# Kernel optimization log

Hardware: AMD Instinct MI355X
Metric: run time of the kernel (lower is better)

Reference implementation:

```python
import jax, jax.numpy as jnp
import numpy as np

N_GRAPHS = 1250
NEG_SLOPE = 0.2

def gat_layer(x, src, dst, W, a_src, a_dst, b, concat):
    # x: [N, Fin]; W: [Fin, H*C]; a_src/a_dst: [H, C]; b: [H*C] or [C]
    N = x.shape[0]
    H, C = a_src.shape
    h = (x @ W).reshape(N, H, C)                      # [N,H,C]
    alpha_s = jnp.sum(h * a_src[None], axis=-1)       # [N,H]
    alpha_d = jnp.sum(h * a_dst[None], axis=-1)       # [N,H]
    e = jax.nn.leaky_relu(alpha_s[src] + alpha_d[dst], NEG_SLOPE)  # [E,H]
    # segment softmax over incoming edges of each target node
    m = jax.ops.segment_max(e, dst, num_segments=N)   # [N,H]
    m = jnp.where(jnp.isfinite(m), m, 0.0)
    ex = jnp.exp(e - m[dst])
    s = jax.ops.segment_sum(ex, dst, num_segments=N)  # [N,H]
    alpha = ex / (s[dst] + 1e-16)                     # [E,H]
    msg = h[src] * alpha[..., None]                   # [E,H,C]
    out = jax.ops.segment_sum(msg, dst, num_segments=N)  # [N,H,C]
    out = out.reshape(N, H * C) if concat else out.mean(axis=1)
    return out + b

def setup_inputs() -> dict:
    key = jax.random.key(0)
    ks = jax.random.split(key, 13)
    N, E = 50000, 100000
    x = jax.random.normal(ks[0], (N, 78), dtype=jnp.float32)
    edge_index = jax.random.randint(ks[1], (2, E), 0, N, dtype=jnp.int64)
    # sorted segment ids -> every graph non-empty (~40 nodes each)
    batch = jnp.sort(jax.random.randint(ks[2], (N,), 0, N_GRAPHS, dtype=jnp.int64))
    g = lambda k, shape, fan: jax.random.normal(k, shape, dtype=jnp.float32) / np.float32(np.sqrt(fan))
    return {
        'x': x, 'edge_index': edge_index, 'batch': batch,
        'W1': g(ks[3], (78, 780), 78), 'a_src1': g(ks[4], (10, 78), 78), 'a_dst1': g(ks[5], (10, 78), 78),
        'b1': jnp.zeros((780,), jnp.float32),
        'W2': g(ks[6], (780, 128), 780), 'a_src2': g(ks[7], (1, 128), 128), 'a_dst2': g(ks[8], (1, 128), 128),
        'b2': jnp.zeros((128,), jnp.float32),
        'fc_w': g(ks[9], (128, 128), 128), 'fc_b': jnp.zeros((128,), jnp.float32),
    }

def reference(x, edge_index, batch, W1, a_src1, a_dst1, b1, W2, a_src2, a_dst2, b2, fc_w, fc_b):
    N = x.shape[0]
    loop = jnp.arange(N, dtype=edge_index.dtype)
    src = jnp.concatenate([edge_index[0], loop])  # add self loops (PyG default)
    dst = jnp.concatenate([edge_index[1], loop])
    # dropout layers are identity in eval mode
    h = jax.nn.elu(gat_layer(x, src, dst, W1, a_src1, a_dst1, b1, concat=True))   # [N,780]
    h = jax.nn.relu(gat_layer(h, src, dst, W2, a_src2, a_dst2, b2, concat=True))  # [N,128]
    g = jax.ops.segment_max(h, batch, num_segments=N_GRAPHS)                      # [G,128]
    g = jnp.where(jnp.isfinite(g), g, 0.0)
    return jax.nn.relu(g @ fc_w + fc_b)
```

## Files before the change

kernel.cpp:

```cpp
#include <hip/hip_runtime.h>
#include <hip/hip_bf16.h>
#include <cstdint>

#define CAP 32
typedef __hip_bfloat16 bf16;
typedef __attribute__((ext_vector_type(8))) short short8;
typedef __attribute__((ext_vector_type(4))) float f32x4;

__device__ __forceinline__ float sb2f(short s) {
  unsigned int u = ((unsigned int)(unsigned short)s) << 16;
  return __uint_as_float(u);
}
__device__ __forceinline__ short f2sb(float f) {
  bf16 h = __float2bfloat16(f);
  return *reinterpret_cast<short*>(&h);
}


__device__ __forceinline__ void edge_sd(const int* __restrict__ ei, int e, int f,
                                        int& src, int& dst) {
  if (e < 100000) {
    if (f) { src = ei[2 * e]; dst = ei[200000 + 2 * e]; }
    else   { src = ei[e];     dst = ei[100000 + e]; }
  } else { src = dst = e - 100000; }
  src = min(max(src, 0), 49999);
  dst = min(max(dst, 0), 49999);
}

__global__ void k_prep(const float* __restrict__ x, const float* __restrict__ W1,
                       const float* __restrict__ W2, const float* __restrict__ aw1,
                       const float* __restrict__ dw1, bf16* __restrict__ xb,
                       bf16* __restrict__ W1t, bf16* __restrict__ W2t,
                       bf16* __restrict__ Wat, float* __restrict__ zp, int zeroWords) {
  int i = blockIdx.x * 256 + threadIdx.x;
  if (i < zeroWords) zp[i] = 0.f;
  const int n_xbv = 50000 * 12;
  const int n_w1 = 832 * 96;
  const int n_w2 = 128 * 832;
  const int n_wa = 32 * 96;
  if (i < n_xbv) {
    int r = i / 12, kg = i - r * 12;
    const float* xr = x + (size_t)r * 78;
    const int k0 = kg * 8;
    short8 ov;
#pragma unroll
    for (int c = 0; c < 8; c++) {
      int k = k0 + c;
      ov[c] = f2sb(k < 78 ? xr[k] : 0.f);
    }
    *(short8*)((short*)xb + (size_t)r * 96 + k0) = ov;
  } else if (i < n_xbv + n_w1) {
    int jdx = i - n_xbv;
    int np = jdx / 96, k = jdx - np * 96;
    int h = np / 80, j = np - h * 80;
    float v = 0.f;
    if (k < 78 && np < 800 && j < 78) v = W1[k * 780 + (h * 78 + j)];
    W1t[jdx] = __float2bfloat16(v);
  } else if (i < n_xbv + n_w1 + n_w2) {
    int jdx = i - n_xbv - n_w1;
    int c = jdx / 832, kp = jdx - c * 832;
    int h = kp / 80, j = kp - h * 80;
    float v = 0.f;
    if (kp < 800 && j < 78) v = W2[(h * 78 + j) * 128 + c];
    W2t[jdx] = __float2bfloat16(v);
  } else if (i < n_xbv + n_w1 + n_w2 + n_wa) {
    int jdx = i - n_xbv - n_w1 - n_w2;
    int c = jdx / 96, k = jdx - c * 96;
    float s = 0.f;
    if (k < 78 && c < 20) {
      const float* w = (c < 10) ? aw1 : dw1;
      int h = (c < 10) ? c : c - 10;
      const float* wrow = W1 + k * 780 + h * 78;
      const float* arow = w + h * 78;
      for (int q = 0; q < 78; q++) s += wrow[q] * arow[q];
    }
    Wat[c * 96 + k] = __float2bfloat16(s);
  }
}

__global__ __launch_bounds__(256) void k_gemm1(const bf16* __restrict__ xb,
                                               const bf16* __restrict__ W1t,
                                               const bf16* __restrict__ Wat,
                                               const float* __restrict__ b1,
                                               bf16* __restrict__ H1,
                                               float* __restrict__ as1,
                                               float* __restrict__ ad1) {
  __shared__ __align__(16) short Als[64 * 104];
  __shared__ __align__(16) short Bls[64 * 104];
  __shared__ __align__(16) short Wls[32 * 104];
  __shared__ __align__(16) float Cls[64 * 68];
  __shared__ float b1s[832];
  const int t = threadIdx.x;
  const int w = t >> 6, l = t & 63, l15 = l & 15, q = l >> 4;
  const int rowBase = blockIdx.x * 64;
  for (int s = t; s < 768; s += 256) {
    int row = s / 12, kg = s - row * 12;
    short8 v = {};
    int gr = rowBase + row;
    if (gr < 50000) v = *(const short8*)((const short*)xb + (size_t)gr * 96 + kg * 8);
    *(short8*)&Als[row * 104 + kg * 8] = v;
  }
  for (int s = t; s < 384; s += 256) {
    int row = s / 12, kg = s - row * 12;
    *(short8*)&Wls[row * 104 + kg * 8] =
        *(const short8*)((const short*)Wat + (size_t)row * 96 + kg * 8);
  }
  for (int s = t; s < 832; s += 256) {
    int h = s / 80, j = s - h * 80;
    b1s[s] = (s < 800 && j < 78) ? b1[h * 78 + j] : 0.f;
  }
  short8 breg[3];
  int bn[3], bk[3];
#pragma unroll
  for (int i = 0; i < 3; i++) {
    int s = t + i * 256;
    bn[i] = s / 12; bk[i] = s - bn[i] * 12;
    breg[i] = *(const short8*)((const short*)W1t + (size_t)bn[i] * 96 + bk[i] * 8);
  }
  for (int cc = 0; cc < 13; cc++) {
    __syncthreads();
#pragma unroll
    for (int i = 0; i < 3; i++) *(short8*)&Bls[bn[i] * 104 + bk[i] * 8] = breg[i];
    if (cc < 12) {
#pragma unroll
      for (int i = 0; i < 3; i++)
        breg[i] = *(const short8*)((const short*)W1t +
                                   (size_t)((cc + 1) * 64 + bn[i]) * 96 + bk[i] * 8);
    }
    __syncthreads();
    f32x4 acc[4] = {};
#pragma unroll
    for (int ks = 0; ks < 3; ks++) {
      short8 a = *(const short8*)&Als[(w * 16 + l15) * 104 + ks * 32 + q * 8];
#pragma unroll
      for (int nt = 0; nt < 4; nt++) {
        short8 b = *(const short8*)&Bls[(nt * 16 + l15) * 104 + ks * 32 + q * 8];
        acc[nt] = __builtin_amdgcn_mfma_f32_16x16x32_bf16(a, b, acc[nt], 0, 0, 0);
      }
    }
    __syncthreads();
#pragma unroll
    for (int nt = 0; nt < 4; nt++)
#pragma unroll
      for (int r = 0; r < 4; r++)
        Cls[(w * 16 + q * 4 + r) * 68 + nt * 16 + l15] = acc[nt][r];
    __syncthreads();
    {
      int r = t >> 2, c0 = (t & 3) * 16;
      int gr = rowBase + r;
      if (gr < 50000) {
        short8 o0, o1;
#pragma unroll
        for (int c = 0; c < 8; c++) o0[c] = f2sb(Cls[r * 68 + c0 + c] + b1s[cc * 64 + c0 + c]);
#pragma unroll
        for (int c = 0; c < 8; c++) o1[c] = f2sb(Cls[r * 68 + c0 + 8 + c] + b1s[cc * 64 + c0 + 8 + c]);
        short* dst = (short*)H1 + (size_t)gr * 832 + cc * 64 + c0;
        *(short8*)dst = o0;
        *(short8*)(dst + 8) = o1;
      }
    }
  }
  f32x4 acc2[2] = {};
#pragma unroll
  for (int ks = 0; ks < 3; ks++) {
    short8 a = *(const short8*)&Als[(w * 16 + l15) * 104 + ks * 32 + q * 8];
#pragma unroll
    for (int nt = 0; nt < 2; nt++) {
      short8 b = *(const short8*)&Wls[(nt * 16 + l15) * 104 + ks * 32 + q * 8];
      acc2[nt] = __builtin_amdgcn_mfma_f32_16x16x32_bf16(a, b, acc2[nt], 0, 0, 0);
    }
  }
  const int gr0 = rowBase + w * 16 + q * 4;
#pragma unroll
  for (int nt = 0; nt < 2; nt++) {
    int c = nt * 16 + l15;
#pragma unroll
    for (int r = 0; r < 4; r++) {
      int gr = gr0 + r;
      if (gr < 50000) {
        if (c < 10)       as1[gr * 10 + c] = acc2[nt][r];
        else if (c < 20)  ad1[gr * 10 + (c - 10)] = acc2[nt][r];
      }
    }
  }
}

__global__ void k_scatter(const int* __restrict__ ei, int* __restrict__ cnt,
                          int* __restrict__ csr, int* __restrict__ flag) {
  __shared__ int sf;
  const int t = threadIdx.x;
  if (t == 0) sf = 0;
  __syncthreads();
  int v = 0;
  for (int i = 1 + 2 * t; i < 2000; i += 512) v |= ei[i];
  if (v) atomicOr(&sf, 1);
  __syncthreads();
  const int f = (sf == 0) ? 1 : 0;
  if (blockIdx.x == 0 && t == 0) flag[0] = f;
  int e = blockIdx.x * 256 + t;
  if (e >= 150000) return;
  int src, dst;
  edge_sd(ei, e, f, src, dst);
  int pos = atomicAdd(&cnt[dst], 1);
  if (pos < CAP) csr[dst * CAP + pos] = src;
}

__global__ __launch_bounds__(256) void k_agg1(const bf16* __restrict__ H1,
                                              const float* __restrict__ as1,
                                              const float* __restrict__ ad1,
                                              const int* __restrict__ csr,
                                              const int* __restrict__ cnt,
                                              bf16* __restrict__ HL2) {
  __shared__ float sexw[2][CAP * 10];
  __shared__ float sden[2][16];
  __shared__ int ssrc[2][CAP];
  __shared__ int scnt[2];
  const int t = threadIdx.x;
  const int sub = t >> 7, tt = t & 127;
  const int n = blockIdx.x * 2 + sub;
  if (t < 2) scnt[t] = min(cnt[blockIdx.x * 2 + t], CAP);
  if (t >= 32 && t < 64) { int z = t - 32; sden[z >> 4][z & 15] = 0.f; }
  __syncthreads();
  const int cn = scnt[sub];
  if (tt < cn) ssrc[sub][tt] = csr[n * CAP + tt];
  __syncthreads();
  for (int wv = tt; wv < cn * 10; wv += 128) {
    int k = wv / 10, h = wv - k * 10;
    int src = ssrc[sub][k];
    float e = as1[src * 10 + h] + ad1[n * 10 + h];
    e = e >= 0.f ? e : 0.2f * e;
    float ex = __expf(e);
    sexw[sub][wv] = ex;
    atomicAdd(&sden[sub][h], ex);
  }
  __syncthreads();
  if (tt < 100) {
    const int head = tt / 10;
    const int j0 = tt * 8;
    float acc[8] = {};
    const float* sw = sexw[sub] + head;
    const short* H1s = (const short*)H1;
    for (int k = 0; k < cn; k++) {
      int src = ssrc[sub][k];
      short8 hv = *(const short8*)(H1s + (size_t)src * 832 + j0);
      float wk = sw[k * 10];
#pragma unroll
      for (int c = 0; c < 8; c++) acc[c] += wk * sb2f(hv[c]);
    }
    const float r0 = 1.f / (sden[sub][head] + 1e-16f);
    short8 ov;
#pragma unroll
    for (int c = 0; c < 8; c++) {
      float v = acc[c] * r0;
      v = v > 0.f ? v : __expf(v) - 1.f;
      ov[c] = f2sb(v);
    }
    *(short8*)((short*)HL2 + (size_t)n * 832 + j0) = ov;
  } else if (tt < 104) {
    short8 z = {};
    *(short8*)((short*)HL2 + (size_t)n * 832 + tt * 8) = z;
  }
}

__global__ __launch_bounds__(256) void k_gemm2(const bf16* __restrict__ A,
                                               const bf16* __restrict__ W2t,
                                               const float* __restrict__ AW2,
                                               const float* __restrict__ DW2,
                                               bf16* __restrict__ H2,
                                               float* __restrict__ as2,
                                               float* __restrict__ ad2) {
  __shared__ __align__(16) short Als[64 * 72];
  __shared__ __align__(16) short Bls[128 * 72];
  __shared__ float sAW[128], sDW[128];
  __shared__ float sS[4][64], sD[4][64];
  const int t = threadIdx.x;
  const int w = t >> 6, l = t & 63, l15 = l & 15, q = l >> 4;
  const int rowBase = blockIdx.x * 64;
  if (t < 128) sAW[t] = AW2[t];
  else         sDW[t - 128] = DW2[t - 128];
  const int ar = t >> 2, ak = t & 3;
  short8 areg[2], breg[4];
  {
    int gr0 = rowBase + ar;
#pragma unroll
    for (int i = 0; i < 2; i++) {
      short8 v = {};
      int gr = gr0;
      if (gr < 50000)
        v = *(const short8*)((const short*)A + (size_t)gr * 832 + 0 + (ak * 2 + i) * 8);
      areg[i] = v;
    }
#pragma unroll
    for (int i = 0; i < 4; i++) {
      int s = t + i * 256;
      int col = s >> 3, kg = s & 7;
      breg[i] = *(const short8*)((const short*)W2t + (size_t)col * 832 + 0 + kg * 8);
    }
  }
  f32x4 acc[4][2] = {};
  for (int kb = 0; kb < 832; kb += 64) {
    __syncthreads();
#pragma unroll
    for (int i = 0; i < 2; i++)
      *(short8*)&Als[ar * 72 + (ak * 2 + i) * 8] = areg[i];
#pragma unroll
    for (int i = 0; i < 4; i++) {
      int s = t + i * 256;
      int col = s >> 3, kg = s & 7;
      *(short8*)&Bls[col * 72 + kg * 8] = breg[i];
    }
    if (kb < 768) {
      int kn = kb + 64;
      int gr = rowBase + ar;
#pragma unroll
      for (int i = 0; i < 2; i++) {
        short8 v = {};
        if (gr < 50000)
          v = *(const short8*)((const short*)A + (size_t)gr * 832 + kn + (ak * 2 + i) * 8);
        areg[i] = v;
      }
#pragma unroll
      for (int i = 0; i < 4; i++) {
        int s = t + i * 256;
        int col = s >> 3, kg = s & 7;
        breg[i] = *(const short8*)((const short*)W2t + (size_t)col * 832 + kn + kg * 8);
      }
    }
    __syncthreads();
#pragma unroll
    for (int ks = 0; ks < 2; ks++) {
      short8 a[4];
#pragma unroll
      for (int mt = 0; mt < 4; mt++)
        a[mt] = *(const short8*)&Als[(mt * 16 + l15) * 72 + ks * 32 + q * 8];
#pragma unroll
      for (int ntl = 0; ntl < 2; ntl++) {
        short8 b = *(const short8*)&Bls[((w * 2 + ntl) * 16 + l15) * 72 + ks * 32 + q * 8];
#pragma unroll
        for (int mt = 0; mt < 4; mt++)
          acc[mt][ntl] = __builtin_amdgcn_mfma_f32_16x16x32_bf16(a[mt], b, acc[mt][ntl], 0, 0, 0);
      }
    }
  }
  const int col0 = w * 32 + l15, col1 = col0 + 16;
  const float aw0 = sAW[col0], aw1 = sAW[col1];
  const float dw0 = sDW[col0], dw1 = sDW[col1];
  f32x4 sp[4], dp[4];
#pragma unroll
  for (int mt = 0; mt < 4; mt++) {
    sp[mt] = acc[mt][0] * aw0 + acc[mt][1] * aw1;
    dp[mt] = acc[mt][0] * dw0 + acc[mt][1] * dw1;
  }
#pragma unroll
  for (int m = 1; m < 16; m <<= 1) {
#pragma unroll
    for (int mt = 0; mt < 4; mt++)
#pragma unroll
      for (int r = 0; r < 4; r++) {
        sp[mt][r] += __shfl_xor(sp[mt][r], m, 64);
        dp[mt][r] += __shfl_xor(dp[mt][r], m, 64);
      }
  }
  if (l15 == 0) {
#pragma unroll
    for (int mt = 0; mt < 4; mt++)
#pragma unroll
      for (int r = 0; r < 4; r++) {
        sS[w][mt * 16 + q * 4 + r] = sp[mt][r];
        sD[w][mt * 16 + q * 4 + r] = dp[mt][r];
      }
  }
#pragma unroll
  for (int mt = 0; mt < 4; mt++) {
    int gr0 = rowBase + mt * 16 + q * 4;
#pragma unroll
    for (int ntl = 0; ntl < 2; ntl++) {
      int gc = w * 32 + ntl * 16 + l15;
#pragma unroll
      for (int r = 0; r < 4; r++) {
        int gr = gr0 + r;
        if (gr < 50000) H2[(size_t)gr * 128 + gc] = __float2bfloat16(acc[mt][ntl][r]);
      }
    }
  }
  __syncthreads();
  if (t < 64) {
    int gr = rowBase + t;
    if (gr < 50000) as2[gr] = sS[0][t] + sS[1][t] + sS[2][t] + sS[3][t];
  } else if (t < 128) {
    int r2 = t - 64;
    int gr = rowBase + r2;
    if (gr < 50000) ad2[gr] = sD[0][r2] + sD[1][r2] + sD[2][r2] + sD[3][r2];
  }
}

__global__ __launch_bounds__(128) void k_agg2(const bf16* __restrict__ H2,
                                              const float* __restrict__ as2,
                                              const float* __restrict__ ad2,
                                              const int* __restrict__ csr,
                                              const int* __restrict__ cnt,
                                              const float* __restrict__ b2,
                                              const int* __restrict__ batch,
                                              const int* __restrict__ flag,
                                              float* __restrict__ g) {
  __shared__ int ssrc[CAP];
  __shared__ float sexw[CAP];
  __shared__ float sden;
  __shared__ int scnt, sbv;
  const int t = threadIdx.x;
  const int n = blockIdx.x;
  if (t == 0) {
    scnt = min(cnt[n], CAP);
    sden = 0.f;
    int b = flag[0] ? batch[2 * n] : batch[n];
    sbv = min(max(b, 0), 1249);
  }
  __syncthreads();
  const int cn = scnt;
  if (t < cn) {
    int src = csr[n * CAP + t];
    ssrc[t] = src;
    float e = as2[src] + ad2[n];
    e = e >= 0.f ? e : 0.2f * e;
    float ex = __expf(e);
    sexw[t] = ex;
    atomicAdd(&sden, ex);
  }
  __syncthreads();
  const short* H2s = (const short*)H2;
  float acc = 0.f;
  if (cn > 0) {
    short hv = H2s[(size_t)ssrc[0] * 128 + t];
    for (int k = 0; k < cn; k++) {
      short hn = hv;
      if (k + 1 < cn) hn = H2s[(size_t)ssrc[k + 1] * 128 + t];
      acc += sexw[k] * sb2f(hv);
      hv = hn;
    }
  }
  float v = acc / (sden + 1e-16f) + b2[t];
  v = v > 0.f ? v : 0.f;
  atomicMax((int*)&g[sbv * 128 + t], __float_as_int(v));
}

__global__ __launch_bounds__(128) void k_fc(const float* __restrict__ g,
                                            const float* __restrict__ fw,
                                            const float* __restrict__ fb,
                                            float* __restrict__ out) {
  const int n = blockIdx.x, t = threadIdx.x;
  __shared__ float grow[128];
  grow[t] = g[n * 128 + t];
  __syncthreads();
  float acc = fb[t];
  for (int k = 0; k < 128; k++) acc += grow[k] * fw[k * 128 + t];
  out[n * 128 + t] = acc > 0.f ? acc : 0.f;
}

extern "C" void kernel_launch(void* const* d_in, const int* in_sizes, int n_in,
                              void* d_out, int out_size, void* d_ws, size_t ws_size,
                              hipStream_t stream) {
  const float* x     = (const float*)d_in[0];
  const int*   ei    = (const int*)d_in[1];
  const int*   batch = (const int*)d_in[2];
  const float* W1    = (const float*)d_in[3];
  const float* as1w  = (const float*)d_in[4];
  const float* ad1w  = (const float*)d_in[5];
  const float* b1    = (const float*)d_in[6];
  const float* W2    = (const float*)d_in[7];
  const float* as2w  = (const float*)d_in[8];
  const float* ad2w  = (const float*)d_in[9];
  const float* b2    = (const float*)d_in[10];
  const float* fcw   = (const float*)d_in[11];
  const float* fcb   = (const float*)d_in[12];
  float* out = (float*)d_out;

  char* p = (char*)d_ws;
  size_t off = 0;
  auto alloc = [&](size_t bytes) -> void* {
    void* r = p + off;
    off = (off + bytes + 15) & ~(size_t)15;
    return r;
  };
  int*   cnt = (int*)  alloc(50000 * 4);
  float* g   = (float*)alloc(160000 * 4);
  size_t zeroWords = off / 4;
  float* as1 = (float*)alloc(500000 * 4);
  float* ad1 = (float*)alloc(500000 * 4);
  float* as2 = (float*)alloc(50000 * 4);
  float* ad2 = (float*)alloc(50000 * 4);
  bf16*  W1t = (bf16*) alloc((size_t)832 * 96 * 2);
  bf16*  W2t = (bf16*) alloc((size_t)128 * 832 * 2);
  bf16*  Wat = (bf16*) alloc((size_t)32 * 96 * 2);
  bf16*  h1  = (bf16*) alloc((size_t)50000 * 832 * 2);
  bf16*  hl2 = (bf16*) alloc((size_t)50000 * 832 * 2);
  int*   csr = (int*)  alloc((size_t)50000 * CAP * 4);
  void*  uni = alloc((size_t)50000 * 128 * 2);
  bf16*  xb  = (bf16*)uni;
  bf16*  h2  = (bf16*)uni;
  int*   flag = (int*) alloc(16);
  (void)ws_size; (void)in_sizes; (void)n_in; (void)out_size;

  int prepN = 50000 * 12 + 832 * 96 + 128 * 832 + 32 * 96;
  k_prep<<<(prepN + 255) / 256, 256, 0, stream>>>(
      x, W1, W2, as1w, ad1w, xb, W1t, W2t, Wat, (float*)d_ws, (int)zeroWords);

  k_gemm1<<<782, 256, 0, stream>>>(xb, W1t, Wat, b1, h1, as1, ad1);
  k_scatter<<<(150000 + 255) / 256, 256, 0, stream>>>(ei, cnt, csr, flag);
  k_agg1<<<25000, 256, 0, stream>>>(h1, as1, ad1, csr, cnt, hl2);
  k_gemm2<<<782, 256, 0, stream>>>(hl2, W2t, as2w, ad2w, h2, as2, ad2);
  k_agg2<<<50000, 128, 0, stream>>>(h2, as2, ad2, csr, cnt, b2, batch, flag, g);
  k_fc<<<1250, 128, 0, stream>>>(g, fcw, fcb, out);
}
```

Measured before the change: 277.1 us.

## Map one wavefront per node in layer-2 aggregation with shuffle-based softmax

The layer-2 aggregation kernel now assigns one 64-lane wavefront per destination node (four nodes per 256-thread block) instead of one 128-thread block per node. The softmax denominator and per-edge weights are shared through wavefront shuffles instead of shared memory, shared atomics and block barriers. Each lane loads two bf16 features at once as a 32-bit word. This cuts the block count, barrier overhead and shared-memory atomics, but each lane now issues twice as many global atomicMax operations.

```diff
diff --git a/kernel.cpp b/kernel.cpp
--- a/kernel.cpp
+++ b/kernel.cpp
@@ -394,7 +394,7 @@
   }
 }
 
-__global__ __launch_bounds__(128) void k_agg2(const bf16* __restrict__ H2,
+__global__ __launch_bounds__(256) void k_agg2(const bf16* __restrict__ H2,
                                               const float* __restrict__ as2,
                                               const float* __restrict__ ad2,
                                               const int* __restrict__ csr,
@@ -403,44 +403,54 @@
                                               const int* __restrict__ batch,
                                               const int* __restrict__ flag,
                                               float* __restrict__ g) {
-  __shared__ int ssrc[CAP];
-  __shared__ float sexw[CAP];
-  __shared__ float sden;
-  __shared__ int scnt, sbv;
   const int t = threadIdx.x;
-  const int n = blockIdx.x;
-  if (t == 0) {
-    scnt = min(cnt[n], CAP);
-    sden = 0.f;
-    int b = flag[0] ? batch[2 * n] : batch[n];
-    sbv = min(max(b, 0), 1249);
-  }
-  __syncthreads();
-  const int cn = scnt;
-  if (t < cn) {
-    int src = csr[n * CAP + t];
-    ssrc[t] = src;
-    float e = as2[src] + ad2[n];
+  const int wid = t >> 6, lane = t & 63;
+  const int n = blockIdx.x * 4 + wid;
+  const int f = flag[0];
+  int b = f ? batch[2 * n] : batch[n];
+  b = min(max(b, 0), 1249);
+  const int cn = min(cnt[n], CAP);
+  int srcv = 0;
+  float exv = 0.f;
+  if (lane < cn) {
+    srcv = csr[n * CAP + lane];
+    float e = as2[srcv] + ad2[n];
     e = e >= 0.f ? e : 0.2f * e;
-    float ex = __expf(e);
-    sexw[t] = ex;
-    atomicAdd(&sden, ex);
-  }
-  __syncthreads();
+    exv = __expf(e);
+  }
+  float den = exv;
+#pragma unroll
+  for (int m = 1; m < 64; m <<= 1) den += __shfl_xor(den, m, 64);
+  const float winv = 1.f / (den + 1e-16f);
   const short* H2s = (const short*)H2;
-  float acc = 0.f;
-  if (cn > 0) {
-    short hv = H2s[(size_t)ssrc[0] * 128 + t];
-    for (int k = 0; k < cn; k++) {
-      short hn = hv;
-      if (k + 1 < cn) hn = H2s[(size_t)ssrc[k + 1] * 128 + t];
-      acc += sexw[k] * sb2f(hv);
-      hv = hn;
-    }
-  }
-  float v = acc / (sden + 1e-16f) + b2[t];
-  v = v > 0.f ? v : 0.f;
-  atomicMax((int*)&g[sbv * 128 + t], __float_as_int(v));
+  float a0 = 0.f, a1 = 0.f;
+  unsigned int hv = 0;
+  float wcur = 0.f;
+  {
+    int s0 = __shfl(srcv, 0, 64);
+    wcur = __shfl(exv, 0, 64);
+    hv = *(const unsigned int*)(H2s + (size_t)s0 * 128 + lane * 2);
+  }
+  for (int k = 1; k <= cn; k++) {
+    unsigned int hn = 0;
+    float wn = 0.f;
+    if (k < cn) {
+      int sk = __shfl(srcv, k, 64);
+      wn = __shfl(exv, k, 64);
+      hn = *(const unsigned int*)(H2s + (size_t)sk * 128 + lane * 2);
+    }
+    a0 += wcur * sb2f((short)(hv & 0xffff));
+    a1 += wcur * sb2f((short)(hv >> 16));
+    hv = hn;
+    wcur = wn;
+  }
+  const int c0 = lane * 2;
+  float v0 = a0 * winv + b2[c0];
+  float v1 = a1 * winv + b2[c0 + 1];
+  v0 = v0 > 0.f ? v0 : 0.f;
+  v1 = v1 > 0.f ? v1 : 0.f;
+  atomicMax((int*)&g[b * 128 + c0], __float_as_int(v0));
+  atomicMax((int*)&g[b * 128 + c0 + 1], __float_as_int(v1));
 }
 
 __global__ __launch_bounds__(128) void k_fc(const float* __restrict__ g,
@@ -508,6 +518,6 @@
   k_scatter<<<(150000 + 255) / 256, 256, 0, stream>>>(ei, cnt, csr, flag);
   k_agg1<<<25000, 256, 0, stream>>>(h1, as1, ad1, csr, cnt, hl2);
   k_gemm2<<<782, 256, 0, stream>>>(hl2, W2t, as2w, ad2w, h2, as2, ad2);
-  k_agg2<<<50000, 128, 0, stream>>>(h2, as2, ad2, csr, cnt, b2, batch, flag, g);
+  k_agg2<<<12500, 256, 0, stream>>>(h2, as2, ad2, csr, cnt, b2, batch, flag, g);
   k_fc<<<1250, 128, 0, stream>>>(g, fcw, fcb, out);
 }
```

New measurement: 278.4 us. No clear change (+0.5%).
